# Optimization experiments

Hardware: AMD Instinct MI355X
Metric: run time of the kernel (lower is better)

Reference implementation:

```python
import jax, jax.numpy as jnp
import numpy as np
from jax import lax

EPS = 1e-5
NUM_GROUPS = 4  # min(4, output_channels)


def setup_inputs() -> dict:
    key = jax.random.key(0)
    ks = jax.random.split(key, 8)
    B, C, T, H, W = 8, 64, 16, 56, 56
    Cout = 128
    return {
        "x": jax.random.normal(ks[0], (B, C, T, H, W), jnp.float32),
        "spatial_w": jax.random.normal(ks[1], (C, 1, 3, 3), jnp.float32) * 0.1,
        "spatial_b": jax.random.normal(ks[2], (C,), jnp.float32) * 0.1,
        "temporal_w": jax.random.normal(ks[3], (C, 1, 3, 1, 1), jnp.float32) * 0.1,
        "temporal_b": jax.random.normal(ks[4], (C,), jnp.float32) * 0.1,
        "pointwise_w": jax.random.normal(ks[5], (Cout, C), jnp.float32) * 0.1,
        "pointwise_b": jax.random.normal(ks[6], (Cout,), jnp.float32) * 0.1,
        "gn_w": jnp.ones((Cout,), jnp.float32),
        "gn_b": jnp.zeros((Cout,), jnp.float32),
    }


def reference(x, spatial_w, spatial_b, temporal_w, temporal_b,
              pointwise_w, pointwise_b, gn_w, gn_b):
    B, C, T, H, W = x.shape
    Cout = pointwise_w.shape[0]

    # Depthwise spatial conv2d: batch the per-frame loop by folding T into N.
    xs = x.transpose(0, 2, 1, 3, 4).reshape(B * T, C, H, W)
    ys = lax.conv_general_dilated(
        xs, spatial_w, window_strides=(1, 1), padding=((1, 1), (1, 1)),
        dimension_numbers=("NCHW", "OIHW", "NCHW"), feature_group_count=C)
    ys = ys + spatial_b[None, :, None, None]
    y = ys.reshape(B, T, C, H, W).transpose(0, 2, 1, 3, 4)  # (B,C,T,H,W)

    # Depthwise temporal conv3d with kernel (3,1,1), padding (1,0,0).
    z = lax.conv_general_dilated(
        y, temporal_w, window_strides=(1, 1, 1),
        padding=((1, 1), (0, 0), (0, 0)),
        dimension_numbers=("NCDHW", "OIDHW", "NCDHW"), feature_group_count=C)
    z = z + temporal_b[None, :, None, None, None]

    # Pointwise 1x1x1 conv == channel GEMM.
    p = jnp.einsum("bcthw,oc->bothw", z, pointwise_w)
    p = p + pointwise_b[None, :, None, None, None]

    # GroupNorm (num_groups=4) + ReLU.
    pg = p.reshape(B, NUM_GROUPS, Cout // NUM_GROUPS, T, H, W)
    mean = pg.mean(axis=(2, 3, 4, 5), keepdims=True)
    var = pg.var(axis=(2, 3, 4, 5), keepdims=True)
    normed = ((pg - mean) * lax.rsqrt(var + EPS)).reshape(B, Cout, T, H, W)
    out = normed * gn_w[None, :, None, None, None] + gn_b[None, :, None, None, None]
    return jax.nn.relu(out)
```

## Files before the change

kernel.cpp:

```cpp
#include <hip/hip_runtime.h>
#include <hip/hip_bf16.h>

#define Bb 8
#define Cc 64
#define Tt 16
#define Hh 56
#define Ww 56
#define COUT 128
#define HW (Hh*Ww)
#define THW (Tt*HW)
#define NPG ((double)(32*THW))

typedef __attribute__((ext_vector_type(8))) short short8v;
typedef __attribute__((ext_vector_type(4))) float f32x4;

__device__ __forceinline__ unsigned short f2bf(float x) {
  __hip_bfloat16 h = __float2bfloat16(x);
  return *reinterpret_cast<unsigned short*>(&h);
}
__device__ __forceinline__ float blo(unsigned int u) {
  return __uint_as_float(u << 16);
}
__device__ __forceinline__ float bhi(unsigned int u) {
  return __uint_as_float(u & 0xFFFF0000u);
}
__device__ __forceinline__ unsigned int pack2(float a, float b) {
  return (unsigned int)f2bf(a) | ((unsigned int)f2bf(b) << 16);
}

__global__ __launch_bounds__(256) void k1_dwconv(
    const float* __restrict__ x,  const float* __restrict__ sw,
    const float* __restrict__ sb, const float* __restrict__ tw,
    const float* __restrict__ tb, unsigned int* __restrict__ zq,
    double* __restrict__ stats)
{
  __shared__ unsigned int raw[HW];
  __shared__ unsigned int ring[3][HW];

  const int tid = threadIdx.x;
  if (blockIdx.x == 0 && tid < 64) stats[tid] = 0.0;

  const int tq = blockIdx.x & 3;
  const int c2 = (blockIdx.x >> 2) & 31;
  const int b  =  blockIdx.x >> 7;
  const int t0 = tq * 4;
  const int ca = c2 * 2, cb = ca + 1;

  float s9a[9], s9b[9];
#pragma unroll
  for (int k = 0; k < 9; ++k) { s9a[k] = sw[ca * 9 + k]; s9b[k] = sw[cb * 9 + k]; }
  float ta3[3], tb3[3];
#pragma unroll
  for (int k = 0; k < 3; ++k) { ta3[k] = tw[ca * 3 + k]; tb3[k] = tw[cb * 3 + k]; }
  const float sba = sb[ca], sbb = sb[cb];
  const float tba = tb[ca], tbb = tb[cb];

  const float* xa = x + (size_t)(b * Cc + ca) * THW;
  const float* xb = x + (size_t)(b * Cc + cb) * THW;
  unsigned int* zbase = zq + (size_t)(b * 32 + c2) * THW;

  for (int tt = t0 - 1; tt <= t0 + 4; ++tt) {
    if (tt >= 0 && tt < Tt) {
      const float* xpa = xa + tt * HW;
      const float* xpb = xb + tt * HW;
      for (int f = tid; f < HW / 4; f += 256) {
        float4 va = *(const float4*)(xpa + f * 4);
        float4 vb = *(const float4*)(xpb + f * 4);
        uint4 pk;
        pk.x = pack2(va.x, vb.x);
        pk.y = pack2(va.y, vb.y);
        pk.z = pack2(va.z, vb.z);
        pk.w = pack2(va.w, vb.w);
        *(uint4*)&raw[f * 4] = pk;
      }
    }
    __syncthreads();

    if (tt >= 0 && tt < Tt) {
      unsigned int* rg = ring[tt % 3];
      for (int q = tid; q < HW / 4; q += 256) {
        int h  = q / 14;
        int w0 = (q - h * 14) * 4;
        float sa0 = sba, sa1 = sba, sa2 = sba, sa3 = sba;
        float sb0 = sbb, sb1 = sbb, sb2 = sbb, sb3 = sbb;
#pragma unroll
        for (int dh = -1; dh <= 1; ++dh) {
          int hh = h + dh;
          if (hh < 0 || hh > Hh - 1) continue;
          const unsigned int* rr = &raw[hh * Ww + w0];
          uint4 mv = *(const uint4*)rr;
          unsigned int lf = (w0 > 0)      ? rr[-1] : 0u;
          unsigned int rt = (w0 < Ww - 4) ? rr[4]  : 0u;
          float am1 = blo(lf),  a0 = blo(mv.x), a1 = blo(mv.y);
          float a2  = blo(mv.z), a3 = blo(mv.w), a4 = blo(rt);
          float bm1 = bhi(lf),  b0 = bhi(mv.x), b1 = bhi(mv.y);
          float b2  = bhi(mv.z), b3 = bhi(mv.w), b4 = bhi(rt);
          float k0a = s9a[(dh + 1) * 3 + 0], k1a = s9a[(dh + 1) * 3 + 1], k2a = s9a[(dh + 1) * 3 + 2];
          float k0b = s9b[(dh + 1) * 3 + 0], k1b = s9b[(dh + 1) * 3 + 1], k2b = s9b[(dh + 1) * 3 + 2];
          sa0 = fmaf(k0a, am1, fmaf(k1a, a0, fmaf(k2a, a1, sa0)));
          sa1 = fmaf(k0a, a0,  fmaf(k1a, a1, fmaf(k2a, a2, sa1)));
          sa2 = fmaf(k0a, a1,  fmaf(k1a, a2, fmaf(k2a, a3, sa2)));
          sa3 = fmaf(k0a, a2,  fmaf(k1a, a3, fmaf(k2a, a4, sa3)));
          sb0 = fmaf(k0b, bm1, fmaf(k1b, b0, fmaf(k2b, b1, sb0)));
          sb1 = fmaf(k0b, b0,  fmaf(k1b, b1, fmaf(k2b, b2, sb1)));
          sb2 = fmaf(k0b, b1,  fmaf(k1b, b2, fmaf(k2b, b3, sb2)));
          sb3 = fmaf(k0b, b2,  fmaf(k1b, b3, fmaf(k2b, b4, sb3)));
        }
        uint4 pk;
        pk.x = pack2(sa0, sb0);
        pk.y = pack2(sa1, sb1);
        pk.z = pack2(sa2, sb2);
        pk.w = pack2(sa3, sb3);
        *(uint4*)&rg[q * 4] = pk;
      }
    }
    __syncthreads();

    int t_out = tt - 1;
    if (t_out >= t0 && t_out <= t0 + 3) {
      unsigned int* zp = zbase + (size_t)t_out * HW;
      for (int q = tid; q < HW / 4; q += 256) {
        float aa0 = tba, aa1 = tba, aa2 = tba, aa3 = tba;
        float bb0 = tbb, bb1 = tbb, bb2 = tbb, bb3 = tbb;
#pragma unroll
        for (int dt = -1; dt <= 1; ++dt) {
          int ti = t_out + dt;
          if (ti < 0 || ti > Tt - 1) continue;
          float tka = ta3[dt + 1], tkb = tb3[dt + 1];
          uint4 v = *(const uint4*)&ring[ti % 3][q * 4];
          aa0 = fmaf(tka, blo(v.x), aa0);  bb0 = fmaf(tkb, bhi(v.x), bb0);
          aa1 = fmaf(tka, blo(v.y), aa1);  bb1 = fmaf(tkb, bhi(v.y), bb1);
          aa2 = fmaf(tka, blo(v.z), aa2);  bb2 = fmaf(tkb, bhi(v.z), bb2);
          aa3 = fmaf(tka, blo(v.w), aa3);  bb3 = fmaf(tkb, bhi(v.w), bb3);
        }
        uint4 o;
        o.x = pack2(aa0, bb0);
        o.y = pack2(aa1, bb1);
        o.z = pack2(aa2, bb2);
        o.w = pack2(aa3, bb3);
        *(uint4*)(zp + q * 4) = o;
      }
    }
    __syncthreads();
  }
}

#define WFRAG_LOAD()                                                           \
  const int lr = tid & 15, lg = (tid >> 4) & 3, wv = tid >> 6;                 \
  const int obase = wv * 32;                                                   \
  short8v wfrag[2][2];                                                         \
  _Pragma("unroll")                                                            \
  for (int ot = 0; ot < 2; ++ot)                                               \
    _Pragma("unroll")                                                          \
    for (int kt = 0; kt < 2; ++kt) {                                           \
      int o  = obase + ot * 16 + lr;                                           \
      int c0 = kt * 32 + lg * 8;                                               \
      float4 wa = *(const float4*)(pw + o * 64 + c0);                          \
      float4 wb = *(const float4*)(pw + o * 64 + c0 + 4);                      \
      short8v fr;                                                              \
      fr[0] = (short)f2bf(wa.x); fr[1] = (short)f2bf(wa.y);                    \
      fr[2] = (short)f2bf(wa.z); fr[3] = (short)f2bf(wa.w);                    \
      fr[4] = (short)f2bf(wb.x); fr[5] = (short)f2bf(wb.y);                    \
      fr[6] = (short)f2bf(wb.z); fr[7] = (short)f2bf(wb.w);                    \
      wfrag[ot][kt] = fr;                                                      \
    }

#define LDT(it, S) {                                                           \
  int p0 = (it) * 128;                                                         \
  _Pragma("unroll")                                                            \
  for (int i = 0; i < 4; ++i) {                                                \
    int f = tid + i * 256; int pos = f & 127; int c2q = f >> 7;                \
    const unsigned int* src = zb + (size_t)(c2q * 4) * THW + p0 + pos;         \
    S[i][0] = src[0];                                                          \
    S[i][1] = src[THW];                                                        \
    S[i][2] = src[2 * THW];                                                    \
    S[i][3] = src[3 * THW];                                                    \
  } }

#define STT(S, bf) {                                                           \
  _Pragma("unroll")                                                            \
  for (int i = 0; i < 4; ++i) {                                                \
    int f = tid + i * 256; int pos = f & 127; int c2q = f >> 7;                \
    *(uint4*)&zt[bf][pos * 36 + c2q * 4] =                                     \
        make_uint4(S[i][0], S[i][1], S[i][2], S[i][3]);                        \
  } }

#define MFMA_TILE(bufidx)                                                      \
  f32x4 acc[2][8];                                                             \
  _Pragma("unroll")                                                            \
  for (int ot = 0; ot < 2; ++ot)                                               \
    _Pragma("unroll")                                                          \
    for (int pt = 0; pt < 8; ++pt) {                                           \
      acc[ot][pt][0] = 0.f; acc[ot][pt][1] = 0.f;                              \
      acc[ot][pt][2] = 0.f; acc[ot][pt][3] = 0.f;                              \
    }                                                                          \
  {                                                                            \
    const unsigned int* ztb = &zt[bufidx][lr * 36 + lg * 4];                   \
    _Pragma("unroll")                                                          \
    for (int kt = 0; kt < 2; ++kt) {                                           \
      _Pragma("unroll")                                                        \
      for (int pt = 0; pt < 8; ++pt) {                                         \
        uint4 zr4 = *(const uint4*)(ztb + pt * (16 * 36) + kt * 16);           \
        union { uint4 u; short8v s; } zfu; zfu.u = zr4;                        \
        acc[0][pt] = __builtin_amdgcn_mfma_f32_16x16x32_bf16(                  \
            zfu.s, wfrag[0][kt], acc[0][pt], 0, 0, 0);                         \
        acc[1][pt] = __builtin_amdgcn_mfma_f32_16x16x32_bf16(                  \
            zfu.s, wfrag[1][kt], acc[1][pt], 0, 0, 0);                         \
      }                                                                        \
    }                                                                          \
  }

#define STATS_BODY()                                                           \
  _Pragma("unroll")                                                            \
  for (int ot = 0; ot < 2; ++ot)                                               \
    _Pragma("unroll")                                                          \
    for (int pt = 0; pt < 8; ++pt)                                             \
      _Pragma("unroll")                                                        \
      for (int r = 0; r < 4; ++r) {                                            \
        float d = acc[ot][pt][r] + pbl[ot];                                    \
        s1 += d;                                                               \
        s2 = fmaf(d, d, s2);                                                   \
      }

__global__ __launch_bounds__(256) void k2_stats(
    const unsigned int* __restrict__ zq, const float* __restrict__ pw,
    const float* __restrict__ pb, double* __restrict__ stats)
{
  __shared__ unsigned int zt[2][128 * 36];
  const int tid = threadIdx.x;
  const int b  = blockIdx.x / 98;
  const int pg = blockIdx.x - b * 98;

  WFRAG_LOAD();
  const float pbl[2] = { pb[obase + lr], pb[obase + 16 + lr] };
  const unsigned int* zb = zq + (size_t)(b * 32) * THW + pg * 512;

  unsigned int st[4][4];
  LDT(0, st); STT(st, 0);

  float s1 = 0.0f, s2 = 0.0f;
  for (int it = 0; it < 4; ++it) {
    __syncthreads();
    if (it < 3) LDT(it + 1, st);
    MFMA_TILE(it & 1);
    if (it < 3) STT(st, (it + 1) & 1);
    STATS_BODY();
  }

#pragma unroll
  for (int off = 32; off; off >>= 1) {
    s1 += __shfl_xor(s1, off);
    s2 += __shfl_xor(s2, off);
  }
  if ((tid & 63) == 0) {
    atomicAdd(&stats[(b * 4 + wv) * 2 + 0], (double)s1);
    atomicAdd(&stats[(b * 4 + wv) * 2 + 1], (double)s2);
  }
}

#define STORE_BODY(itn)                                                        \
  _Pragma("unroll")                                                            \
  for (int ot = 0; ot < 2; ++ot) {                                             \
    int o = obase + ot * 16 + lr;                                              \
    float A = Ac[ot], B = Bc[ot];                                              \
    float* orow = ob + (size_t)o * THW + (itn) * 128;                          \
    _Pragma("unroll")                                                          \
    for (int pt = 0; pt < 8; ++pt) {                                           \
      f32x4 a = acc[ot][pt];                                                   \
      float4 v;                                                                \
      v.x = fmaf(a[0], A, B); v.x = v.x > 0.0f ? v.x : 0.0f;                   \
      v.y = fmaf(a[1], A, B); v.y = v.y > 0.0f ? v.y : 0.0f;                   \
      v.z = fmaf(a[2], A, B); v.z = v.z > 0.0f ? v.z : 0.0f;                   \
      v.w = fmaf(a[3], A, B); v.w = v.w > 0.0f ? v.w : 0.0f;                   \
      *(float4*)(orow + pt * 16) = v;                                          \
    }                                                                          \
  }

__global__ __launch_bounds__(256) void k3_norm(
    const unsigned int* __restrict__ zq, const float* __restrict__ pw,
    const float* __restrict__ pb, const double* __restrict__ stats,
    const float* __restrict__ gnw, const float* __restrict__ gnb,
    float* __restrict__ out)
{
  __shared__ unsigned int zt[2][128 * 36];
  const int tid = threadIdx.x;
  const int b  = blockIdx.x / 98;
  const int pg = blockIdx.x - b * 98;

  WFRAG_LOAD();

  double sm1 = stats[(b * 4 + wv) * 2 + 0];
  double sm2 = stats[(b * 4 + wv) * 2 + 1];
  double md = sm1 / NPG;
  double vd = sm2 / NPG - md * md;
  float m   = (float)md;
  float inv = rsqrtf((float)vd + 1e-5f);

  float Ac[2], Bc[2];
#pragma unroll
  for (int ot = 0; ot < 2; ++ot) {
    int o = obase + ot * 16 + lr;
    float A = inv * gnw[o];
    Ac[ot] = A;
    Bc[ot] = fmaf(pb[o] - m, A, gnb[o]);
  }

  const unsigned int* zb = zq + (size_t)(b * 32) * THW + pg * 512;
  float* ob = out + (size_t)(b * COUT) * THW + pg * 512 + lg * 4;

  unsigned int st[4][4];
  LDT(0, st); STT(st, 0);

  for (int it = 0; it < 4; ++it) {
    __syncthreads();
    if (it < 3) LDT(it + 1, st);
    MFMA_TILE(it & 1);
    if (it < 3) STT(st, (it + 1) & 1);
    STORE_BODY(it);
  }
}

extern "C" void kernel_launch(void* const* d_in, const int* in_sizes, int n_in,
                              void* d_out, int out_size, void* d_ws, size_t ws_size,
                              hipStream_t stream)
{
  const float* x   = (const float*)d_in[0];
  const float* sw  = (const float*)d_in[1];
  const float* sb  = (const float*)d_in[2];
  const float* tw  = (const float*)d_in[3];
  const float* tb  = (const float*)d_in[4];
  const float* pw  = (const float*)d_in[5];
  const float* pb  = (const float*)d_in[6];
  const float* gnw = (const float*)d_in[7];
  const float* gnb = (const float*)d_in[8];
  float* out = (float*)d_out;

  double* stats    = (double*)d_ws;
  unsigned int* zq = (unsigned int*)((char*)d_ws + 512);

  k1_dwconv<<<Bb * 32 * 4, 256, 0, stream>>>(x, sw, sb, tw, tb, zq, stats);
  k2_stats<<<Bb * 98, 256, 0, stream>>>(zq, pw, pb, stats);
  k3_norm <<<Bb * 98, 256, 0, stream>>>(zq, pw, pb, stats, gnw, gnb, out);
}
```

Measured before the change: 156.2 us.

## Fuse temporal conv into spatial pass with register accumulators, drop LDS ring

Removes the 3-frame shared-memory ring of spatial-conv outputs and instead carries the temporal conv as per-thread register accumulators (accP/accC) over the four work items each thread owns. Each spatial result is folded straight into the running temporal sums, and a z frame is written once its third tap arrives. This drops one __syncthreads per frame, the LDS write/read round trip, and one bf16 rounding of the intermediate. In exchange it adds 64 float registers per thread, which may lower occupancy.

```diff
diff --git a/kernel.cpp b/kernel.cpp
--- a/kernel.cpp
+++ b/kernel.cpp
@@ -35,7 +35,6 @@
     double* __restrict__ stats)
 {
   __shared__ unsigned int raw[HW];
-  __shared__ unsigned int ring[3][HW];
 
   const int tid = threadIdx.x;
   if (blockIdx.x == 0 && tid < 64) stats[tid] = 0.0;
@@ -49,9 +48,8 @@
   float s9a[9], s9b[9];
 #pragma unroll
   for (int k = 0; k < 9; ++k) { s9a[k] = sw[ca * 9 + k]; s9b[k] = sw[cb * 9 + k]; }
-  float ta3[3], tb3[3];
-#pragma unroll
-  for (int k = 0; k < 3; ++k) { ta3[k] = tw[ca * 3 + k]; tb3[k] = tw[cb * 3 + k]; }
+  const float tw0a = tw[ca * 3 + 0], tw1a = tw[ca * 3 + 1], tw2a = tw[ca * 3 + 2];
+  const float tw0b = tw[cb * 3 + 0], tw1b = tw[cb * 3 + 1], tw2b = tw[cb * 3 + 2];
   const float sba = sb[ca], sbb = sb[cb];
   const float tba = tb[ca], tbb = tb[cb];
 
@@ -59,86 +57,103 @@
   const float* xb = x + (size_t)(b * Cc + cb) * THW;
   unsigned int* zbase = zq + (size_t)(b * 32 + c2) * THW;
 
-  for (int tt = t0 - 1; tt <= t0 + 4; ++tt) {
-    if (tt >= 0 && tt < Tt) {
+  float accP[4][8], accC[4][8];
+#pragma unroll
+  for (int i = 0; i < 4; ++i)
+#pragma unroll
+    for (int j = 0; j < 8; ++j) { accP[i][j] = 0.f; accC[i][j] = 0.f; }
+
+  for (int k = 0; k < 6; ++k) {
+    const int tt = t0 - 1 + k;
+    const bool val = (tt >= 0 && tt < Tt);
+
+    if (val) {
       const float* xpa = xa + tt * HW;
       const float* xpb = xb + tt * HW;
-      for (int f = tid; f < HW / 4; f += 256) {
-        float4 va = *(const float4*)(xpa + f * 4);
-        float4 vb = *(const float4*)(xpb + f * 4);
-        uint4 pk;
-        pk.x = pack2(va.x, vb.x);
-        pk.y = pack2(va.y, vb.y);
-        pk.z = pack2(va.z, vb.z);
-        pk.w = pack2(va.w, vb.w);
-        *(uint4*)&raw[f * 4] = pk;
+#pragma unroll
+      for (int i = 0; i < 4; ++i) {
+        int f = tid + i * 256;
+        if (f < HW / 4) {
+          float4 va = *(const float4*)(xpa + f * 4);
+          float4 vb = *(const float4*)(xpb + f * 4);
+          uint4 pk;
+          pk.x = pack2(va.x, vb.x);
+          pk.y = pack2(va.y, vb.y);
+          pk.z = pack2(va.z, vb.z);
+          pk.w = pack2(va.w, vb.w);
+          *(uint4*)&raw[f * 4] = pk;
+        }
       }
     }
     __syncthreads();
 
-    if (tt >= 0 && tt < Tt) {
-      unsigned int* rg = ring[tt % 3];
-      for (int q = tid; q < HW / 4; q += 256) {
-        int h  = q / 14;
-        int w0 = (q - h * 14) * 4;
-        float sa0 = sba, sa1 = sba, sa2 = sba, sa3 = sba;
-        float sb0 = sbb, sb1 = sbb, sb2 = sbb, sb3 = sbb;
-#pragma unroll
-        for (int dh = -1; dh <= 1; ++dh) {
-          int hh = h + dh;
-          if (hh < 0 || hh > Hh - 1) continue;
-          const unsigned int* rr = &raw[hh * Ww + w0];
-          uint4 mv = *(const uint4*)rr;
-          unsigned int lf = (w0 > 0)      ? rr[-1] : 0u;
-          unsigned int rt = (w0 < Ww - 4) ? rr[4]  : 0u;
-          float am1 = blo(lf),  a0 = blo(mv.x), a1 = blo(mv.y);
-          float a2  = blo(mv.z), a3 = blo(mv.w), a4 = blo(rt);
-          float bm1 = bhi(lf),  b0 = bhi(mv.x), b1 = bhi(mv.y);
-          float b2  = bhi(mv.z), b3 = bhi(mv.w), b4 = bhi(rt);
-          float k0a = s9a[(dh + 1) * 3 + 0], k1a = s9a[(dh + 1) * 3 + 1], k2a = s9a[(dh + 1) * 3 + 2];
-          float k0b = s9b[(dh + 1) * 3 + 0], k1b = s9b[(dh + 1) * 3 + 1], k2b = s9b[(dh + 1) * 3 + 2];
-          sa0 = fmaf(k0a, am1, fmaf(k1a, a0, fmaf(k2a, a1, sa0)));
-          sa1 = fmaf(k0a, a0,  fmaf(k1a, a1, fmaf(k2a, a2, sa1)));
-          sa2 = fmaf(k0a, a1,  fmaf(k1a, a2, fmaf(k2a, a3, sa2)));
-          sa3 = fmaf(k0a, a2,  fmaf(k1a, a3, fmaf(k2a, a4, sa3)));
-          sb0 = fmaf(k0b, bm1, fmaf(k1b, b0, fmaf(k2b, b1, sb0)));
-          sb1 = fmaf(k0b, b0,  fmaf(k1b, b1, fmaf(k2b, b2, sb1)));
-          sb2 = fmaf(k0b, b1,  fmaf(k1b, b2, fmaf(k2b, b3, sb2)));
-          sb3 = fmaf(k0b, b2,  fmaf(k1b, b3, fmaf(k2b, b4, sb3)));
+    const bool emit = (k >= 2);
+    const int t_out = tt - 1;
+    unsigned int* zp = zbase + (size_t)t_out * HW;
+
+#pragma unroll
+    for (int i = 0; i < 4; ++i) {
+      int q = tid + i * 256;
+      if (q < HW / 4) {
+        float s[8];
+        if (val) {
+          int h  = q / 14;
+          int w0 = (q - h * 14) * 4;
+          float sa0 = sba, sa1 = sba, sa2 = sba, sa3 = sba;
+          float sb0 = sbb, sb1 = sbb, sb2 = sbb, sb3 = sbb;
+#pragma unroll
+          for (int dh = -1; dh <= 1; ++dh) {
+            int hh = h + dh;
+            if (hh < 0 || hh > Hh - 1) continue;
+            const unsigned int* rr = &raw[hh * Ww + w0];
+            uint4 mv = *(const uint4*)rr;
+            unsigned int lf = (w0 > 0)      ? rr[-1] : 0u;
+            unsigned int rt = (w0 < Ww - 4) ? rr[4]  : 0u;
+            float am1 = blo(lf),  a0 = blo(mv.x), a1 = blo(mv.y);
+            float a2  = blo(mv.z), a3 = blo(mv.w), a4 = blo(rt);
+            float bm1 = bhi(lf),  b0 = bhi(mv.x), b1 = bhi(mv.y);
+            float b2  = bhi(mv.z), b3 = bhi(mv.w), b4 = bhi(rt);
+            float k0a = s9a[(dh + 1) * 3 + 0], k1a = s9a[(dh + 1) * 3 + 1], k2a = s9a[(dh + 1) * 3 + 2];
+            float k0b = s9b[(dh + 1) * 3 + 0], k1b = s9b[(dh + 1) * 3 + 1], k2b = s9b[(dh + 1) * 3 + 2];
+            sa0 = fmaf(k0a, am1, fmaf(k1a, a0, fmaf(k2a, a1, sa0)));
+            sa1 = fmaf(k0a, a0,  fmaf(k1a, a1, fmaf(k2a, a2, sa1)));
+            sa2 = fmaf(k0a, a1,  fmaf(k1a, a2, fmaf(k2a, a3, sa2)));
+            sa3 = fmaf(k0a, a2,  fmaf(k1a, a3, fmaf(k2a, a4, sa3)));
+            sb0 = fmaf(k0b, bm1, fmaf(k1b, b0, fmaf(k2b, b1, sb0)));
+            sb1 = fmaf(k0b, b0,  fmaf(k1b, b1, fmaf(k2b, b2, sb1)));
+            sb2 = fmaf(k0b, b1,  fmaf(k1b, b2, fmaf(k2b, b3, sb2)));
+            sb3 = fmaf(k0b, b2,  fmaf(k1b, b3, fmaf(k2b, b4, sb3)));
+          }
+          s[0] = sa0; s[1] = sa1; s[2] = sa2; s[3] = sa3;
+          s[4] = sb0; s[5] = sb1; s[6] = sb2; s[7] = sb3;
+        } else {
+#pragma unroll
+          for (int j = 0; j < 8; ++j) s[j] = 0.0f;
         }
-        uint4 pk;
-        pk.x = pack2(sa0, sb0);
-        pk.y = pack2(sa1, sb1);
-        pk.z = pack2(sa2, sb2);
-        pk.w = pack2(sa3, sb3);
-        *(uint4*)&rg[q * 4] = pk;
-      }
-    }
-    __syncthreads();
-
-    int t_out = tt - 1;
-    if (t_out >= t0 && t_out <= t0 + 3) {
-      unsigned int* zp = zbase + (size_t)t_out * HW;
-      for (int q = tid; q < HW / 4; q += 256) {
-        float aa0 = tba, aa1 = tba, aa2 = tba, aa3 = tba;
-        float bb0 = tbb, bb1 = tbb, bb2 = tbb, bb3 = tbb;
-#pragma unroll
-        for (int dt = -1; dt <= 1; ++dt) {
-          int ti = t_out + dt;
-          if (ti < 0 || ti > Tt - 1) continue;
-          float tka = ta3[dt + 1], tkb = tb3[dt + 1];
-          uint4 v = *(const uint4*)&ring[ti % 3][q * 4];
-          aa0 = fmaf(tka, blo(v.x), aa0);  bb0 = fmaf(tkb, bhi(v.x), bb0);
-          aa1 = fmaf(tka, blo(v.y), aa1);  bb1 = fmaf(tkb, bhi(v.y), bb1);
-          aa2 = fmaf(tka, blo(v.z), aa2);  bb2 = fmaf(tkb, bhi(v.z), bb2);
-          aa3 = fmaf(tka, blo(v.w), aa3);  bb3 = fmaf(tkb, bhi(v.w), bb3);
+
+        if (emit) {
+          float z0 = fmaf(tw2a, s[0], accP[i][0]);
+          float z1 = fmaf(tw2a, s[1], accP[i][1]);
+          float z2 = fmaf(tw2a, s[2], accP[i][2]);
+          float z3 = fmaf(tw2a, s[3], accP[i][3]);
+          float z4 = fmaf(tw2b, s[4], accP[i][4]);
+          float z5 = fmaf(tw2b, s[5], accP[i][5]);
+          float z6 = fmaf(tw2b, s[6], accP[i][6]);
+          float z7 = fmaf(tw2b, s[7], accP[i][7]);
+          uint4 o;
+          o.x = pack2(z0, z4);
+          o.y = pack2(z1, z5);
+          o.z = pack2(z2, z6);
+          o.w = pack2(z3, z7);
+          *(uint4*)(zp + q * 4) = o;
         }
-        uint4 o;
-        o.x = pack2(aa0, bb0);
-        o.y = pack2(aa1, bb1);
-        o.z = pack2(aa2, bb2);
-        o.w = pack2(aa3, bb3);
-        *(uint4*)(zp + q * 4) = o;
+#pragma unroll
+        for (int j = 0; j < 4; ++j) {
+          accP[i][j]     = fmaf(tw1a, s[j],     accC[i][j]);
+          accP[i][j + 4] = fmaf(tw1b, s[j + 4], accC[i][j + 4]);
+          accC[i][j]     = fmaf(tw0a, s[j],     tba);
+          accC[i][j + 4] = fmaf(tw0b, s[j + 4], tbb);
+        }
       }
     }
     __syncthreads();
```

Measured after the change: 147.5 us. -5.6%, faster.
